# Kernel optimization log

Measured on AMD Instinct MI355X. Metric: run time of the kernel, lower is better.

## Reference

```python
import jax, jax.numpy as jnp
import numpy as np

EPS = 1e-16

def setup_inputs() -> dict:
    key = jax.random.key(0)
    k1, k2 = jax.random.split(key)
    lhs = jax.random.uniform(k1, (100000, 2), dtype=jnp.float32)
    rhs = jax.random.uniform(k2, (512, 2), dtype=jnp.float32)
    return {"lhs": lhs, "rhs": rhs}

def reference(lhs, rhs):
    # lhs: [N,2] (w,h), rhs: [M,2] (w,h) -> IoU matrix [N,M]
    lw, lh = lhs[:, 0:1], lhs[:, 1:2]          # [N,1]
    rw, rh = rhs[None, :, 0], rhs[None, :, 1]  # [1,M]
    intersection = jnp.minimum(lw, rw) * jnp.minimum(lh, rh)   # [N,M]
    union = lw * lh + rw * rh - intersection                    # [N,M]
    return intersection / union + EPS
```

## Files before the change

kernel.cpp:

```cpp
#include <hip/hip_runtime.h>


#define NCOLS 512
#define COLS4 (NCOLS / 4)

__global__ __launch_bounds__(256) void iou_kernel(
    const float2* __restrict__ lhs,
    const float2* __restrict__ rhs,
    float* __restrict__ out,
    int total4)
{
    int idx4 = blockIdx.x * blockDim.x + threadIdx.x;
    if (idx4 >= total4) return;

    int i  = idx4 >> 7;
    int j4 = (idx4 & (COLS4 - 1)) << 2;

    float2 l = lhs[i];
    float la = l.x * l.y;

    const float4* rhs4 = (const float4*)rhs;
    float4 rA = rhs4[j4 >> 1];
    float4 rB = rhs4[(j4 >> 1) + 1];

    float rw[4] = {rA.x, rA.z, rB.x, rB.z};
    float rh[4] = {rA.y, rA.w, rB.y, rB.w};

    float res[4];
#pragma unroll
    for (int k = 0; k < 4; ++k) {
        float inter = fminf(l.x, rw[k]) * fminf(l.y, rh[k]);
        float uni   = fmaf(rw[k], rh[k], la) - inter;
        res[k] = inter * __builtin_amdgcn_rcpf(uni) + 1e-16f;
    }

    float4 o = make_float4(res[0], res[1], res[2], res[3]);
    ((float4*)out)[idx4] = o;
}

extern "C" void kernel_launch(void* const* d_in, const int* in_sizes, int n_in,
                              void* d_out, int out_size, void* d_ws, size_t ws_size,
                              hipStream_t stream) {
    const float2* lhs = (const float2*)d_in[0];
    const float2* rhs = (const float2*)d_in[1];
    float* out = (float*)d_out;

    int n_lhs  = in_sizes[0] / 2;
    int total4 = n_lhs * (NCOLS / 4);

    int block = 256;
    int grid  = (total4 + block - 1) / block;
    iou_kernel<<<grid, block, 0, stream>>>(lhs, rhs, out, total4);
}
```

Before: 218.7 us.

## Use persistent wave-per-row loop with register-cached rhs and nontemporal stores

```diff
diff --git a/kernel.cpp b/kernel.cpp
--- a/kernel.cpp
+++ b/kernel.cpp
@@ -2,53 +2,61 @@
 
 
 #define NCOLS 512
-#define COLS4 (NCOLS / 4)
+
+typedef float vfloat4 __attribute__((ext_vector_type(4)));
 
 __global__ __launch_bounds__(256) void iou_kernel(
     const float2* __restrict__ lhs,
-    const float2* __restrict__ rhs,
+    const float*  __restrict__ rhs,
     float* __restrict__ out,
-    int total4)
+    int n_rows, int total_waves)
 {
-    int idx4 = blockIdx.x * blockDim.x + threadIdx.x;
-    if (idx4 >= total4) return;
+    const int tid  = blockIdx.x * blockDim.x + threadIdx.x;
+    const int lane = threadIdx.x & 63;
+    const int wave = __builtin_amdgcn_readfirstlane(tid >> 6);
 
-    int i  = idx4 >> 7;
-    int j4 = (idx4 & (COLS4 - 1)) << 2;
+    const vfloat4* rhs4 = (const vfloat4*)rhs;
+    vfloat4 a0 = rhs4[2 * lane];
+    vfloat4 a1 = rhs4[2 * lane + 1];
+    vfloat4 b0 = rhs4[128 + 2 * lane];
+    vfloat4 b1 = rhs4[128 + 2 * lane + 1];
 
-    float2 l = lhs[i];
-    float la = l.x * l.y;
+    float rw[8] = {a0.x, a0.z, a1.x, a1.z, b0.x, b0.z, b1.x, b1.z};
+    float rh[8] = {a0.y, a0.w, a1.y, a1.w, b0.y, b0.w, b1.y, b1.w};
+    float ra[8];
+#pragma unroll
+    for (int k = 0; k < 8; ++k) ra[k] = rw[k] * rh[k];
 
-    const float4* rhs4 = (const float4*)rhs;
-    float4 rA = rhs4[j4 >> 1];
-    float4 rB = rhs4[(j4 >> 1) + 1];
+    for (int row = wave; row < n_rows; row += total_waves) {
+        float2 l = lhs[row];
+        float la = l.x * l.y;
 
-    float rw[4] = {rA.x, rA.z, rB.x, rB.z};
-    float rh[4] = {rA.y, rA.w, rB.y, rB.w};
+        float o[8];
+#pragma unroll
+        for (int k = 0; k < 8; ++k) {
+            float inter = fminf(l.x, rw[k]) * fminf(l.y, rh[k]);
+            float uni   = (la + ra[k]) - inter;
+            o[k] = fmaf(inter, __builtin_amdgcn_rcpf(uni), 1e-16f);
+        }
 
-    float res[4];
-#pragma unroll
-    for (int k = 0; k < 4; ++k) {
-        float inter = fminf(l.x, rw[k]) * fminf(l.y, rh[k]);
-        float uni   = fmaf(rw[k], rh[k], la) - inter;
-        res[k] = inter * __builtin_amdgcn_rcpf(uni) + 1e-16f;
+        vfloat4* orow = (vfloat4*)(out + (size_t)row * NCOLS);
+        vfloat4 v0 = {o[0], o[1], o[2], o[3]};
+        vfloat4 v1 = {o[4], o[5], o[6], o[7]};
+        __builtin_nontemporal_store(v0, orow + lane);
+        __builtin_nontemporal_store(v1, orow + 64 + lane);
     }
-
-    float4 o = make_float4(res[0], res[1], res[2], res[3]);
-    ((float4*)out)[idx4] = o;
 }
 
 extern "C" void kernel_launch(void* const* d_in, const int* in_sizes, int n_in,
                               void* d_out, int out_size, void* d_ws, size_t ws_size,
                               hipStream_t stream) {
     const float2* lhs = (const float2*)d_in[0];
-    const float2* rhs = (const float2*)d_in[1];
+    const float*  rhs = (const float*)d_in[1];
     float* out = (float*)d_out;
 
-    int n_lhs  = in_sizes[0] / 2;
-    int total4 = n_lhs * (NCOLS / 4);
+    int n_rows = in_sizes[0] / 2;
 
-    int block = 256;
-    int grid  = (total4 + block - 1) / block;
-    iou_kernel<<<grid, block, 0, stream>>>(lhs, rhs, out, total4);
+    int blocks = 2048;
+    int total_waves = blocks * (256 / 64);
+    iou_kernel<<<blocks, 256, 0, stream>>>(lhs, rhs, out, n_rows, total_waves);
 }
```

Measured after the change: 210.7 us. -3.7%, faster.
